# Optimization experiments

Hardware: AMD Instinct MI355X
Metric: run time of the kernel (lower is better)

Reference implementation:

```python
import jax, jax.numpy as jnp
import numpy as np

N = 100000   # particles
D = 100      # grid cells per dimension


def setup_inputs() -> dict:
    rng = np.random.default_rng(0)
    d = 0.05  # cell_size in source
    # distinct cells (module assumes one particle per cell)
    cells = rng.choice(D ** 3, size=N, replace=False)
    cz = cells // (D * D)
    cy = (cells // D) % D
    cx = cells % D
    jit = rng.uniform(-0.3, 0.3, size=(3, N)) * d  # |jitter| < 0.5*d keeps round(pos/d)==cell
    x = cx * d + jit[0]
    y = cy * d + jit[1]
    z = cz * d + jit[2]
    v = rng.standard_normal((3, N)) * 0.1
    kn = 60000.0
    restitution = 0.5
    alpha = -np.log(restitution) / np.pi
    gamma = alpha / np.sqrt(alpha ** 2 + 1.0)
    rho_p = 2700.0
    particle_mass = 4.0 / 3.0 * 3.1415 * d ** 3 * rho_p
    eta = 2.0 * gamma * np.sqrt(kn * particle_mass / 2.0)
    return {
        "compressed_x_grid": jnp.asarray(x, jnp.float32),
        "compressed_y_grid": jnp.asarray(y, jnp.float32),
        "compressed_z_grid": jnp.asarray(z, jnp.float32),
        "compressed_vx_grid": jnp.asarray(v[0], jnp.float32),
        "compressed_vy_grid": jnp.asarray(v[1], jnp.float32),
        "compressed_vz_grid": jnp.asarray(v[2], jnp.float32),
        "d": float(d),
        "kn": float(kn),
        "damping_coefficient_Eta": float(eta),
        "friction_coefficient": 0.5,
        "dt": 0.001,
        "input_shape": D,
        "filter_size": 5,
    }


def _forces(x, y, z, vx, vy, vz, d, kn, eta, grid_dim, filter_size):
    n = x.shape[0]
    eps = 1e-4
    # cell indices exactly as in the torch code: round(pos/d)
    cx = jnp.round(x / d).astype(jnp.int32)
    cy = jnp.round(y / d).astype(jnp.int32)
    cz = jnp.round(z / d).astype(jnp.int32)
    # dense particle-index grid; -1 = empty (replaces mask + particle_number_tensor)
    idx = -jnp.ones((grid_dim, grid_dim, grid_dim), jnp.int32)
    idx = idx.at[cz, cy, cx].set(jnp.arange(n, dtype=jnp.int32))
    # all filter_size^3 roll offsets; torch.roll wraps, so use modular indexing
    r = filter_size // 2
    ar = jnp.arange(-r, r + 1)
    off = jnp.stack(jnp.meshgrid(ar, ar, ar, indexing="ij"), axis=-1).reshape(-1, 3)  # [K,3] (sz,sy,sx)
    # pair (A at cell c) with (B at cell c - s): mask_contact_A==2 <=> occ[c] & occ[c-s]
    nz = (cz[:, None] - off[None, :, 0]) % grid_dim  # [N,K]
    ny = (cy[:, None] - off[None, :, 1]) % grid_dim
    nx = (cx[:, None] - off[None, :, 2]) % grid_dim
    B = idx[nz, ny, nx]                                   # [N,K] neighbor particle id or -1
    me = jnp.arange(n, dtype=jnp.int32)[:, None]
    valid = (B >= 0) & (B != me)                          # filters empty cells and self pairs (A != B)
    Bs = jnp.where(valid, B, 0)
    dxp = x[:, None] - x[Bs]
    dyp = y[:, None] - y[Bs]
    dzp = z[:, None] - z[Bs]
    dvx = vx[:, None] - vx[Bs]
    dvy = vy[:, None] - vy[Bs]
    dvz = vz[:, None] - vz[Bs]
    dist = jnp.sqrt(dxp * dxp + dyp * dyp + dzp * dzp)
    denom = jnp.maximum(eps, dist)
    contact = valid & (dist < 2.0 * d)
    # spring (collision) force on A, aggregated over neighbors (row-sum == scatter_add to A)
    coef = jnp.where(contact, kn * (dist - 2.0 * d) / denom, 0.0)
    fx_c = (coef * dxp).sum(axis=1)
    fy_c = (coef * dyp).sum(axis=1)
    fz_c = (coef * dzp).sum(axis=1)
    # normal damping force
    vn = (dvx * dxp + dvy * dyp + dvz * dzp) / denom
    dcoef = jnp.where(contact, eta * vn / denom, 0.0)
    fx_d = (dcoef * dxp).sum(axis=1)
    fy_d = (dcoef * dyp).sum(axis=1)
    fz_d = (dcoef * dzp).sum(axis=1)
    return jnp.stack([fx_c, fy_c, fz_c, fx_d, fy_d, fz_d])  # [6, N]


def reference(compressed_x_grid, compressed_y_grid, compressed_z_grid, compressed_vx_grid, compressed_vy_grid, compressed_vz_grid, d, kn, damping_coefficient_Eta, friction_coefficient, dt, input_shape, filter_size):
    return _forces(compressed_x_grid, compressed_y_grid, compressed_z_grid,
                   compressed_vx_grid, compressed_vy_grid, compressed_vz_grid,
                   d, kn, damping_coefficient_Eta, input_shape, filter_size)
```

## Files before the change

### kernel.cpp

```cpp
#include <hip/hip_runtime.h>

static const int DG = 100;
static const int NCELL = DG * DG * DG;

__global__ __launch_bounds__(256) void scatter_kernel(
    const float* __restrict__ x, const float* __restrict__ y, const float* __restrict__ z,
    const float* __restrict__ dptr, int* __restrict__ cell_idx, int n)
{
    int i = blockIdx.x * blockDim.x + threadIdx.x;
    if (i >= n) return;
    float inv_d = 1.0f / dptr[0];
    int cx = (int)roundf(x[i] * inv_d);
    int cy = (int)roundf(y[i] * inv_d);
    int cz = (int)roundf(z[i] * inv_d);
    cell_idx[(cz * DG + cy) * DG + cx] = i;
}

__global__ __launch_bounds__(256) void force_kernel(
    const float* __restrict__ x, const float* __restrict__ y, const float* __restrict__ z,
    const float* __restrict__ vx, const float* __restrict__ vy, const float* __restrict__ vz,
    const float* __restrict__ dptr, const float* __restrict__ knptr,
    const float* __restrict__ etaptr,
    const int* __restrict__ cell_idx, float* __restrict__ out, int n)
{
    int wid  = blockIdx.x * (blockDim.x >> 6) + (threadIdx.x >> 6);
    if (wid >= n) return;
    int lane = threadIdx.x & 63;
    int p = wid;

    float d    = dptr[0];
    float kn   = knptr[0];
    float eta  = etaptr[0];
    float inv_d = 1.0f / d;
    float two_d = 2.0f * d;

    float px = x[p], py = y[p], pz = z[p];
    float pvx = vx[p], pvy = vy[p], pvz = vz[p];
    int cx = (int)roundf(px * inv_d);
    int cy = (int)roundf(py * inv_d);
    int cz = (int)roundf(pz * inv_d);

    float fxc = 0.f, fyc = 0.f, fzc = 0.f;
    float fxd = 0.f, fyd = 0.f, fzd = 0.f;

    #pragma unroll
    for (int t = 0; t < 2; ++t) {
        int k = lane + t * 64;
        if (k < 125) {
            int sz  = k / 25;
            int rem = k - sz * 25;
            int sy  = rem / 5;
            int sx  = rem - sy * 5;
            int nz = cz - (sz - 2); if (nz < 0) nz += DG; else if (nz >= DG) nz -= DG;
            int ny = cy - (sy - 2); if (ny < 0) ny += DG; else if (ny >= DG) ny -= DG;
            int nx = cx - (sx - 2); if (nx < 0) nx += DG; else if (nx >= DG) nx -= DG;
            int B = cell_idx[(nz * DG + ny) * DG + nx];
            if (B >= 0 && B != p) {
                float dxp = px - x[B];
                float dyp = py - y[B];
                float dzp = pz - z[B];
                float dist = sqrtf(dxp * dxp + dyp * dyp + dzp * dzp);
                if (dist < two_d) {
                    float denom   = fmaxf(1e-4f, dist);
                    float inv_den = 1.0f / denom;
                    float coef = kn * (dist - two_d) * inv_den;
                    fxc += coef * dxp; fyc += coef * dyp; fzc += coef * dzp;
                    float dvxp = pvx - vx[B];
                    float dvyp = pvy - vy[B];
                    float dvzp = pvz - vz[B];
                    float vn    = (dvxp * dxp + dvyp * dyp + dvzp * dzp) * inv_den;
                    float dcoef = eta * vn * inv_den;
                    fxd += dcoef * dxp; fyd += dcoef * dyp; fzd += dcoef * dzp;
                }
            }
        }
    }

    #pragma unroll
    for (int off = 32; off >= 1; off >>= 1) {
        fxc += __shfl_xor(fxc, off, 64);
        fyc += __shfl_xor(fyc, off, 64);
        fzc += __shfl_xor(fzc, off, 64);
        fxd += __shfl_xor(fxd, off, 64);
        fyd += __shfl_xor(fyd, off, 64);
        fzd += __shfl_xor(fzd, off, 64);
    }

    if (lane == 0) {
        out[p]         = fxc;
        out[n + p]     = fyc;
        out[2 * n + p] = fzc;
        out[3 * n + p] = fxd;
        out[4 * n + p] = fyd;
        out[5 * n + p] = fzd;
    }
}

extern "C" void kernel_launch(void* const* d_in, const int* in_sizes, int n_in,
                              void* d_out, int out_size, void* d_ws, size_t ws_size,
                              hipStream_t stream)
{
    const float* x     = (const float*)d_in[0];
    const float* y     = (const float*)d_in[1];
    const float* z     = (const float*)d_in[2];
    const float* vx    = (const float*)d_in[3];
    const float* vy    = (const float*)d_in[4];
    const float* vz    = (const float*)d_in[5];
    const float* dptr  = (const float*)d_in[6];
    const float* knptr = (const float*)d_in[7];
    const float* etap  = (const float*)d_in[8];
    int n = in_sizes[0];

    int* cell_idx = (int*)d_ws;
    hipMemsetAsync(cell_idx, 0xFF, (size_t)NCELL * sizeof(int), stream);

    int sblocks = (n + 255) / 256;
    scatter_kernel<<<sblocks, 256, 0, stream>>>(x, y, z, dptr, cell_idx, n);

    const int waves_per_block = 4;
    int fblocks = (n + waves_per_block - 1) / waves_per_block;
    force_kernel<<<fblocks, 256, 0, stream>>>(x, y, z, vx, vy, vz,
                                              dptr, knptr, etap,
                                              cell_idx, (float*)d_out, n);
}
```

Measured before the change: 140.9 us.

## Pad cell grid by two to drop periodic wrap and hoist neighbor loads

```diff
diff --git a/kernel.cpp b/kernel.cpp
--- a/kernel.cpp
+++ b/kernel.cpp
@@ -1,7 +1,10 @@
 #include <hip/hip_runtime.h>
 
 static const int DG = 100;
-static const int NCELL = DG * DG * DG;
+static const int PGD = DG + 4;
+static const int PPLANE = PGD * PGD;
+static const int PCELLS = PGD * PGD * PGD;
+
 
 __global__ __launch_bounds__(256) void scatter_kernel(
     const float* __restrict__ x, const float* __restrict__ y, const float* __restrict__ z,
@@ -13,7 +16,7 @@
     int cx = (int)roundf(x[i] * inv_d);
     int cy = (int)roundf(y[i] * inv_d);
     int cz = (int)roundf(z[i] * inv_d);
-    cell_idx[(cz * DG + cy) * DG + cx] = i;
+    cell_idx[((cz + 2) * PGD + (cy + 2)) * PGD + (cx + 2)] = i;
 }
 
 __global__ __launch_bounds__(256) void force_kernel(
@@ -26,7 +29,7 @@
     int wid  = blockIdx.x * (blockDim.x >> 6) + (threadIdx.x >> 6);
     if (wid >= n) return;
     int lane = threadIdx.x & 63;
-    int p = wid;
+    int p = __builtin_amdgcn_readfirstlane(wid);
 
     float d    = dptr[0];
     float kn   = knptr[0];
@@ -39,39 +42,47 @@
     int cx = (int)roundf(px * inv_d);
     int cy = (int)roundf(py * inv_d);
     int cz = (int)roundf(pz * inv_d);
+    int base = ((cz + 2) * PGD + (cy + 2)) * PGD + (cx + 2);
+    base = __builtin_amdgcn_readfirstlane(base);
+    const int* __restrict__ g = cell_idx + base;
+
+    int k1 = lane;
+    int sz = k1 / 25; int r = k1 - sz * 25; int sy = r / 5; int sx = r - sy * 5;
+    int off1 = (sz - 2) * PPLANE + (sy - 2) * PGD + (sx - 2);
+    int k2 = lane + 64;
+    bool has2 = (k2 < 125);
+    int off2 = 0;
+    if (has2) {
+        sz = k2 / 25; r = k2 - sz * 25; sy = r / 5; sx = r - sy * 5;
+        off2 = (sz - 2) * PPLANE + (sy - 2) * PGD + (sx - 2);
+    }
+
+    int B1 = g[off1];
+    int B2 = has2 ? g[off2] : -1;
 
     float fxc = 0.f, fyc = 0.f, fzc = 0.f;
     float fxd = 0.f, fyd = 0.f, fzd = 0.f;
 
     #pragma unroll
     for (int t = 0; t < 2; ++t) {
-        int k = lane + t * 64;
-        if (k < 125) {
-            int sz  = k / 25;
-            int rem = k - sz * 25;
-            int sy  = rem / 5;
-            int sx  = rem - sy * 5;
-            int nz = cz - (sz - 2); if (nz < 0) nz += DG; else if (nz >= DG) nz -= DG;
-            int ny = cy - (sy - 2); if (ny < 0) ny += DG; else if (ny >= DG) ny -= DG;
-            int nx = cx - (sx - 2); if (nx < 0) nx += DG; else if (nx >= DG) nx -= DG;
-            int B = cell_idx[(nz * DG + ny) * DG + nx];
-            if (B >= 0 && B != p) {
-                float dxp = px - x[B];
-                float dyp = py - y[B];
-                float dzp = pz - z[B];
-                float dist = sqrtf(dxp * dxp + dyp * dyp + dzp * dzp);
-                if (dist < two_d) {
-                    float denom   = fmaxf(1e-4f, dist);
-                    float inv_den = 1.0f / denom;
-                    float coef = kn * (dist - two_d) * inv_den;
-                    fxc += coef * dxp; fyc += coef * dyp; fzc += coef * dzp;
-                    float dvxp = pvx - vx[B];
-                    float dvyp = pvy - vy[B];
-                    float dvzp = pvz - vz[B];
-                    float vn    = (dvxp * dxp + dvyp * dyp + dvzp * dzp) * inv_den;
-                    float dcoef = eta * vn * inv_den;
-                    fxd += dcoef * dxp; fyd += dcoef * dyp; fzd += dcoef * dzp;
-                }
+        int B = (t == 0) ? B1 : B2;
+        if (B >= 0 && B != p) {
+            float dxp = px - x[B];
+            float dyp = py - y[B];
+            float dzp = pz - z[B];
+            float d2 = dxp * dxp + dyp * dyp + dzp * dzp;
+            float dist = __builtin_amdgcn_sqrtf(d2);
+            if (dist < two_d) {
+                float denom   = fmaxf(1e-4f, dist);
+                float inv_den = __builtin_amdgcn_rcpf(denom);
+                float coef = kn * (dist - two_d) * inv_den;
+                fxc += coef * dxp; fyc += coef * dyp; fzc += coef * dzp;
+                float dvxp = pvx - vx[B];
+                float dvyp = pvy - vy[B];
+                float dvzp = pvz - vz[B];
+                float vn    = (dvxp * dxp + dvyp * dyp + dvzp * dzp) * inv_den;
+                float dcoef = eta * vn * inv_den;
+                fxd += dcoef * dxp; fyd += dcoef * dyp; fzd += dcoef * dzp;
             }
         }
     }
@@ -86,13 +97,13 @@
         fzd += __shfl_xor(fzd, off, 64);
     }
 
-    if (lane == 0) {
-        out[p]         = fxc;
-        out[n + p]     = fyc;
-        out[2 * n + p] = fzc;
-        out[3 * n + p] = fxd;
-        out[4 * n + p] = fyd;
-        out[5 * n + p] = fzd;
+    if (lane < 6) {
+        float v = (lane == 0) ? fxc
+                : (lane == 1) ? fyc
+                : (lane == 2) ? fzc
+                : (lane == 3) ? fxd
+                : (lane == 4) ? fyd : fzd;
+        out[lane * n + p] = v;
     }
 }
 
@@ -112,7 +123,7 @@
     int n = in_sizes[0];
 
     int* cell_idx = (int*)d_ws;
-    hipMemsetAsync(cell_idx, 0xFF, (size_t)NCELL * sizeof(int), stream);
+    hipMemsetAsync(cell_idx, 0xFF, (size_t)PCELLS * sizeof(int), stream);
 
     int sblocks = (n + 255) / 256;
     scatter_kernel<<<sblocks, 256, 0, stream>>>(x, y, z, dptr, cell_idx, n);
```

Result: faster. 136.2 us (-3.3%).
